# Kernel optimization log

Hardware: AMD Instinct MI355X
Metric: run time of the kernel (lower is better)

The kernel has to match this reference:

```python
import jax, jax.numpy as jnp
import numpy as np

NODE_NUM = 6
C_IN = 1024
B = 16384
N_OPS = 9
TAU = 10.0
EPS = 1e-5
ACTS = (jax.nn.relu, jax.nn.sigmoid, jnp.tanh)


def setup_inputs() -> dict:
    key = jax.random.key(0)
    k = jax.random.split(key, 12)
    n_edges = NODE_NUM * (NODE_NUM + 1) // 2  # 21
    nB = n_edges - NODE_NUM  # 15 edges with cin=cout=C_IN//2

    def w(kk, shape, fan_in):
        return jax.random.normal(kk, shape, jnp.float32) / np.float32(np.sqrt(fan_in))

    return {
        "x": jax.random.normal(k[0], (B, C_IN), jnp.float32),
        "arch_params": 0.001 * jax.random.normal(k[1], (n_edges, N_OPS), jnp.float32),
        "gumbel": jax.random.gumbel(k[2], (n_edges, N_OPS), jnp.float32),
        "dense_w_A": w(k[3], (NODE_NUM, 3, C_IN // 2, C_IN), C_IN),
        "dense_b_A": 0.01 * jax.random.normal(k[4], (NODE_NUM, 3, C_IN // 2), jnp.float32),
        "group_w_A": w(k[5], (NODE_NUM, 3, 4, C_IN // 8, C_IN // 4), C_IN // 4),
        "group_b_A": 0.01 * jax.random.normal(k[6], (NODE_NUM, 3, C_IN // 2), jnp.float32),
        "pool_w_A": w(k[7], (NODE_NUM, 2, C_IN // 2, C_IN), C_IN),
        "dense_w_B": w(k[8], (nB, 3, C_IN // 2, C_IN // 2), C_IN // 2),
        "dense_b_B": 0.01 * jax.random.normal(k[9], (nB, 3, C_IN // 2), jnp.float32),
        "group_w_B": w(k[10], (nB, 3, 4, C_IN // 8, C_IN // 8), C_IN // 8),
        "group_b_B": 0.01 * jax.random.normal(k[11], (nB, 3, C_IN // 2), jnp.float32),
    }


def _batchnorm(h):
    # training-mode BatchNorm2d on [B, C, 1, 1] == normalize over batch, affine-free
    m = jnp.mean(h, axis=0, keepdims=True)
    v = jnp.var(h, axis=0, keepdims=True)
    return (h - m) * jax.lax.rsqrt(v + EPS)


def _apply_edge(h, op_idx, wscale, dw, db, gw, gb, pw):
    # h: [B, cin]; dw: [3, cout, cin]; gw: [3, 4, cout//4, cin//4]; pw: [2, cout, cin] or None
    cout = dw.shape[1]

    def pool(p):
        def f(hh):
            # ReLU-Conv1x1-BN preprocess when cin != cout, else identity
            y = _batchnorm(jax.nn.relu(hh) @ pw[p].T) if pw is not None else hh
            if p == 0:  # avg_pool_3x3 on 1x1 spatial, pad=1, count_include_pad
                y = y / 9.0
            # p == 1: max_pool_3x3 on 1x1 spatial is identity
            return _batchnorm(y)  # MixedOp-appended BatchNorm2d(affine=False)
        return f

    def dense(a):
        return lambda hh: ACTS[a](hh @ dw[a].T + db[a])

    def gdense(a):
        def f(hh):
            hg = hh.reshape(hh.shape[0], 4, -1)  # [B, 4, cin//4]
            y = jnp.einsum('bgi,goi->bgo', hg, gw[a]).reshape(hh.shape[0], -1) + gb[a]
            return ACTS[a](y)
        return f

    zero = lambda hh: jnp.zeros((hh.shape[0], cout), hh.dtype)
    branches = [pool(0), pool(1), dense(0), dense(1), dense(2),
                gdense(0), gdense(1), gdense(2), zero]
    return jax.lax.switch(op_idx, branches, h) * wscale


def reference(x, arch_params, gumbel, dense_w_A, dense_b_A, group_w_A, group_b_A,
              pool_w_A, dense_w_B, dense_b_B, group_w_B, group_b_B):
    # GDAS gumbel-softmax hard routing (straight-through)
    logits = (jax.nn.log_softmax(arch_params, axis=1) + gumbel) / TAU
    prob = jax.nn.softmax(logits, axis=1)
    index = jnp.argmax(prob, axis=1)                      # [n_edges]
    one_h = jax.nn.one_hot(index, N_OPS, dtype=prob.dtype)
    hardwts = one_h - jax.lax.stop_gradient(prob) + prob  # [n_edges, N_OPS]

    # arch rows are indexed by sorted edge-key order, matching torch edge2index
    keys = sorted('{}->{}'.format(j, i + 1) for i in range(NODE_NUM) for j in range(i + 1))
    e2i = {kk: n for n, kk in enumerate(keys)}

    states = [x]
    a_ct = 0
    b_ct = 0
    for i in range(1, NODE_NUM + 1):
        acc = None
        for j in range(i):
            e = e2i['{}->{}'.format(j, i)]
            w_e = hardwts[e, index[e]]
            if j == 0:
                out = _apply_edge(states[0], index[e], w_e, dense_w_A[a_ct], dense_b_A[a_ct],
                                  group_w_A[a_ct], group_b_A[a_ct], pool_w_A[a_ct])
                a_ct += 1
            else:
                out = _apply_edge(states[j], index[e], w_e, dense_w_B[b_ct], dense_b_B[b_ct],
                                  group_w_B[b_ct], group_b_B[b_ct], None)
                b_ct += 1
            acc = out if acc is None else acc + out
        states.append(acc)
    return states[-1]  # [B, C_IN//2]; final_linear is never applied in forward()
```

## Files before the change

kernel.cpp:

```cpp
#include <hip/hip_runtime.h>

#define BATCH 16384
#define CH 512
#define EPSBN 1e-5f

typedef __attribute__((ext_vector_type(8))) short short8;
typedef __attribute__((ext_vector_type(4))) float f32x4;
typedef __attribute__((ext_vector_type(4))) unsigned short ushort4v;

#define GLOAD16(gp, lp) __builtin_amdgcn_global_load_lds( \
    (const __attribute__((address_space(1))) void*)(gp),  \
    (__attribute__((address_space(3))) void*)(lp), 16, 0, 0)

__constant__ int d_etab[6][6] = {
  {0,0,0,0,0,0},
  {1,6,0,0,0,0},
  {2,7,11,0,0,0},
  {3,8,12,15,0,0},
  {4,9,13,16,18,0},
  {5,10,14,17,19,20}};
__constant__ int d_bct[21] = {0,0,0,0,0,0, 0,1,3,6,10, 2,4,7,11, 5,8,12, 9,13, 14};

static __device__ __forceinline__ long woff(int e){
  return (e < 6) ? (long)e*524288 : 3145728L + (long)d_bct[e]*262144;
}

static __device__ __forceinline__ unsigned short f2b(float f){
  union { float f; unsigned u; } v; v.f = f;
  unsigned r = v.u + 0x7fffu + ((v.u >> 16) & 1u);
  return (unsigned short)(r >> 16);
}
static __device__ __forceinline__ float b2f(unsigned short u){
  union { unsigned u; float f; } v; v.u = ((unsigned)u) << 16; return v.f;
}
static __device__ __forceinline__ float actf(int act, float v){
  if (act == 0) return fmaxf(v, 0.f);
  if (act == 1) return 1.f/(1.f + __expf(-v));
  float e = __expf(2.f*v);
  return 1.f - 2.f/(e + 1.f);
}

static __device__ __forceinline__ void col_stats_atomic(
    float vs, float vq, int cn, int slot, float* partw){
  vs += __shfl_xor(vs, 16); vs += __shfl_xor(vs, 32);
  vq += __shfl_xor(vq, 16); vq += __shfl_xor(vq, 32);
  if (((threadIdx.x) & 63) < 16){
    atomicAdd(&partw[((long)slot*CH + cn)*2    ], vs);
    atomicAdd(&partw[((long)slot*CH + cn)*2 + 1], vq);
  }
}

static __device__ __forceinline__ void ms_from(const float* part, int slot, int cn,
                                               float& mu, float& var){
  long sl = ((long)slot*CH + cn)*2;
  float s = part[sl], q = part[sl+1];
  mu = s * (1.f/16384.f);
  var = fmaxf(q * (1.f/16384.f) - mu*mu, 0.f);
}
static __device__ __forceinline__ float alphaA(int id, float v){
  float s1r = rsqrtf(v + EPSBN);
  float vz = v / (v + EPSBN);
  return (id==0) ? (s1r * (1.f/9.f) * rsqrtf(vz*(1.f/81.f) + EPSBN))
                 : (s1r * rsqrtf(vz + EPSBN));
}
static __device__ __forceinline__ float alphaB(int id, float v){
  return (id==0) ? ((1.f/9.f) * rsqrtf(v*(1.f/81.f) + EPSBN))
                 : rsqrtf(v + EPSBN);
}

__global__ void k_sentinel(float* out){ out[0] = 1.0e6f; }

__global__ void k_index(const float* __restrict__ ap, const float* __restrict__ gum,
                        int* __restrict__ idx, float* __restrict__ wsc,
                        int* __restrict__ statNeed){
  __shared__ int sid[21];
  int e = threadIdx.x;
  if (e < 21){
    const float* a = ap + e*9;
    const float* g = gum + e*9;
    float m = a[0];
    for (int o=1;o<9;o++) m = fmaxf(m, a[o]);
    float s = 0.f;
    for (int o=0;o<9;o++) s += expf(a[o]-m);
    float lse = m + logf(s);
    float lg[9]; float lm = -1e30f;
    for (int o=0;o<9;o++){ lg[o] = (a[o]-lse+g[o]) / 10.0f; lm = fmaxf(lm, lg[o]); }
    float ss = 0.f;
    for (int o=0;o<9;o++) ss += expf(lg[o]-lm);
    int bi = 0; float bp = -1.f;
    for (int o=0;o<9;o++){
      float p = expf(lg[o]-lm)/ss;
      if (p > bp){ bp = p; bi = o; }
    }
    idx[e] = bi;
    wsc[e] = (1.0f - bp) + bp;
    sid[e] = bi;
  }
  __syncthreads();
  if (e < 12){
    int need = 0;
    if (e < 6){
      need = (sid[e] < 2) ? 1 : 0;
    } else {
      int j = e - 6;
      if (j >= 1){
        for (int n = j+1; n <= 6; ++n)
          if (sid[d_etab[n-1][j]] < 2) need = 1;
      }
    }
    statNeed[e] = need;
  }
}

__global__ void k_f2b4(const float* __restrict__ in, unsigned short* __restrict__ outp, long n4){
  long stride = (long)gridDim.x*blockDim.x;
  for (long i = (long)blockIdx.x*blockDim.x + threadIdx.x; i < n4; i += stride){
    const float4 v = ((const float4*)in)[i];
    ushort4v o;
    o[0] = f2b(v.x); o[1] = f2b(v.y); o[2] = f2b(v.z); o[3] = f2b(v.w);
    ((ushort4v*)outp)[i] = o;
  }
}

__global__ void k_wconv_all(const int* __restrict__ idxp,
                            const float* __restrict__ dwA, const float* __restrict__ pwA,
                            const float* __restrict__ gwA, const float* __restrict__ dwB,
                            const float* __restrict__ gwB,
                            unsigned short* __restrict__ Wball){
  int e = blockIdx.x >> 7;
  int blk = blockIdx.x & 127;
  int id = idxp[e];
  const float* src; long n;
  if (e < 6){
    int a = e;
    if (id >= 2 && id <= 4){ n = 524288; src = dwA + ((long)a*3 + (id-2))*n; }
    else if (id < 2)       { n = 524288; src = pwA + ((long)a*2 + id)*n; }
    else if (id <= 7)      { n = 131072; src = gwA + ((long)a*3 + (id-5))*131072; }
    else return;
  } else {
    int b = d_bct[e];
    if (id >= 2 && id <= 4)     { n = 262144; src = dwB + ((long)b*3 + (id-2))*n; }
    else if (id >= 5 && id <= 7){ n = 65536;  src = gwB + ((long)b*3 + (id-5))*65536; }
    else return;
  }
  unsigned short* dst = Wball + woff(e);
  long n4 = n >> 2;
  long stride = 128*256;
  for (long i = (long)blk*256 + threadIdx.x; i < n4; i += stride){
    const float4 v = ((const float4*)src)[i];
    ushort4v o;
    o[0] = f2b(v.x); o[1] = f2b(v.y); o[2] = f2b(v.z); o[3] = f2b(v.w);
    ((ushort4v*)dst)[i] = o;
  }
}

__global__ __launch_bounds__(512, 4) void k_gemmA_all(
    const unsigned short* __restrict__ xb, const unsigned short* __restrict__ Wball,
    unsigned short* __restrict__ s0, unsigned short* __restrict__ s1,
    unsigned short* __restrict__ s2, unsigned short* __restrict__ s3,
    unsigned short* __restrict__ s4, unsigned short* __restrict__ pre6,
    const float* __restrict__ dbA, const float* __restrict__ gbA,
    const int* __restrict__ idxp, const float* __restrict__ wscp,
    float* __restrict__ partw)
{
  int e = blockIdx.x >> 9;
  int id = idxp[e];
  if (id == 8) return;
  unsigned short* target;
  switch(e){ case 0: target=s0; break; case 1: target=s1; break; case 2: target=s2; break;
             case 3: target=s3; break; case 4: target=s4; break; default: target=pre6; }
  bool pool = (id < 2);
  bool grp = (id >= 5);
  int K = grp ? 256 : 1024;
  int act = pool ? 0 : (grp ? id-5 : id-2);
  float we = wscp[e];

  int inner = blockIdx.x & 511;
  int lg = (inner & 7) * 64 + (inner >> 3);
  int rowTile = lg >> 2, colTile = lg & 3;
  int row0 = rowTile * 128, col0 = colTile * 128;

  int t = threadIdx.x;
  int lane = t & 63, wave = t >> 6;
  int wm = wave >> 2, wn = wave & 3;
  int l16 = lane & 15, lq = lane >> 4;

  __shared__ unsigned short LDS[24576];

  int ra = t >> 2;
  int ca = (((t & 3) ^ ((ra >> 1) & 3)) << 3);
  int aoff[4], boff[2];
  #pragma unroll
  for (int m=0;m<4;m++){ int R = wm*64 + m*16 + l16; aoff[m] = R*32 + ((lq ^ ((R>>1)&3))<<3); }
  #pragma unroll
  for (int n=0;n<2;n++){ int C = wn*32 + n*16 + l16; boff[n] = C*32 + ((lq ^ ((C>>1)&3))<<3); }

  const unsigned short* Abase = xb + (grp ? (long)colTile*K : 0);
  const unsigned short* Wbase = Wball + (long)e*524288 + (long)col0*K;
  const unsigned short* gA = Abase + (long)(row0 + ra)*1024 + ca;
  const unsigned short* gB = Wbase + (long)ra*K + ca;
  const float* bias = (grp ? gbA : dbA) + ((long)e*3 + act)*CH;

  f32x4 acc[4][2];
  #pragma unroll
  for (int m=0;m<4;m++){ acc[m][0]=(f32x4){0,0,0,0}; acc[m][1]=(f32x4){0,0,0,0}; }

  auto STAGE = [&](int tile, int bsel){
    long kk = (long)tile*32;
    GLOAD16(gA + kk, &LDS[bsel*4096 + t*8]);
    GLOAD16(gB + kk, &LDS[12288 + bsel*4096 + t*8]);
  };

  int nk = K >> 5;
  STAGE(0, 0);
  STAGE(1, 1);
  int cb = 0;
  for (int kt = 0; kt < nk; ++kt){
    if (kt+1 < nk) { asm volatile("s_waitcnt vmcnt(2)" ::: "memory"); }
    else           { asm volatile("s_waitcnt vmcnt(0)" ::: "memory"); }
    __builtin_amdgcn_s_barrier();
    if (kt+2 < nk) STAGE(kt+2, (cb >= 1) ? cb-1 : cb+2);
    const unsigned short* pA = &LDS[cb*4096];
    const unsigned short* pB = &LDS[12288 + cb*4096];
    short8 a[4], b[2];
    #pragma unroll
    for (int m=0;m<4;m++){
      a[m] = *(const short8*)(pA + aoff[m]);
      if (pool){
        #pragma unroll
        for (int q=0;q<8;q++) a[m][q] = (a[m][q] < (short)0) ? (short)0 : a[m][q];
      }
    }
    #pragma unroll
    for (int n=0;n<2;n++) b[n] = *(const short8*)(pB + boff[n]);
    #pragma unroll
    for (int m=0;m<4;m++)
      #pragma unroll
      for (int n=0;n<2;n++)
        acc[m][n] = __builtin_amdgcn_mfma_f32_16x16x32_bf16(a[m], b[n], acc[m][n], 0,0,0);
    cb = (cb+1 == 3) ? 0 : cb+1;
  }

  #pragma unroll
  for (int n=0;n<2;n++){
    int cn = col0 + wn*32 + n*16 + l16;
    float bv = pool ? 0.f : bias[cn];
    float cs = 0.f, cq = 0.f;
    #pragma unroll
    for (int m=0;m<4;m++)
      #pragma unroll
      for (int r=0;r<4;r++){
        int row = row0 + wm*64 + m*16 + lq*4 + r;
        long off = (long)row*CH + cn;
        float v = pool ? acc[m][n][r] : (we * actf(act, acc[m][n][r] + bv));
        target[off] = f2b(v);
        cs += v; cq += v*v;
      }
    if (pool) col_stats_atomic(cs, cq, cn, e, partw);
  }
}

__global__ __launch_bounds__(512, 4) void k_fix1(
    unsigned short* __restrict__ s1, const float* __restrict__ part,
    float* __restrict__ partw, const int* __restrict__ idxp,
    const float* __restrict__ wscp, const int* __restrict__ statNeed)
{
  int id = idxp[0];
  int needS = statNeed[7];
  if (id >= 2 && id != 8 && !needS) return;
  float we = wscp[0];

  int bid = blockIdx.x;
  int lg = (bid & 7) * 64 + (bid >> 3);
  int rowTile = lg >> 2, colTile = lg & 3;
  int row0 = rowTile * 128, col0 = colTile * 128;

  int t = threadIdx.x;
  int lane = t & 63, wave = t >> 6;
  int wm = wave >> 2, wn = wave & 3;
  int l16 = lane & 15, lq = lane >> 4;

  #pragma unroll
  for (int n=0;n<2;n++){
    int cn = col0 + wn*32 + n*16 + l16;
    float cs = 0.f, cq = 0.f;
    float mu = 0.f, al = 0.f;
    if (id < 2){
      float var; ms_from(part, 0, cn, mu, var);
      al = alphaA(id, var);
    }
    #pragma unroll
    for (int m=0;m<4;m++)
      #pragma unroll
      for (int r=0;r<4;r++){
        int row = row0 + wm*64 + m*16 + lq*4 + r;
        long off = (long)row*CH + cn;
        float v;
        if (id == 8){ v = 0.f; s1[off] = 0; }
        else if (id < 2){ v = we * (b2f(s1[off]) - mu) * al; s1[off] = f2b(v); }
        else { v = b2f(s1[off]); }
        cs += v; cq += v*v;
      }
    if (needS) col_stats_atomic(cs, cq, cn, 6+1, partw);
  }
}

__global__ __launch_bounds__(512, 4) void k_fused(
    int node,
    const unsigned short* __restrict__ pre,
    const unsigned short* __restrict__ sb0, const unsigned short* __restrict__ sb1,
    const unsigned short* __restrict__ sb2, const unsigned short* __restrict__ sb3,
    const unsigned short* __restrict__ sb4,
    unsigned short* __restrict__ sbout, float* __restrict__ outf,
    const unsigned short* __restrict__ Wball,
    const float* __restrict__ dbB, const float* __restrict__ gbB,
    const float* __restrict__ part, float* __restrict__ partw,
    const int* __restrict__ idxp, const float* __restrict__ wscp,
    const int* __restrict__ statNeed)
{
  int bid = blockIdx.x;
  int lg = (bid & 7) * 64 + (bid >> 3);
  int rowTile = lg >> 2, colTile = lg & 3;
  int row0 = rowTile * 128, col0 = colTile * 128;

  int t = threadIdx.x;
  int lane = t & 63, wave = t >> 6;
  int wm = wave >> 2, wn = wave & 3;
  int l16 = lane & 15, lq = lane >> 4;

  __shared__ unsigned short LDS[24576];

  int ra = t >> 2;
  int ca = (((t & 3) ^ ((ra >> 1) & 3)) << 3);
  int aoff[4], boff[2];
  #pragma unroll
  for (int m=0;m<4;m++){ int R = wm*64 + m*16 + l16; aoff[m] = R*32 + ((lq ^ ((R>>1)&3))<<3); }
  #pragma unroll
  for (int n=0;n<2;n++){ int C = wn*32 + n*16 + l16; boff[n] = C*32 + ((lq ^ ((C>>1)&3))<<3); }

  f32x4 facc[4][2];
  #pragma unroll
  for (int m=0;m<4;m++){ facc[m][0]=(f32x4){0,0,0,0}; facc[m][1]=(f32x4){0,0,0,0}; }

  for (int jj = 0; jj < node; ++jj){
    int e = d_etab[node-1][jj];
    int id = idxp[e];
    if (id == 8) continue;
    float we = wscp[e];

    if (jj == 0){
      if (id < 2){
        #pragma unroll
        for (int n=0;n<2;n++){
          int cn = col0 + wn*32 + n*16 + l16;
          float mu, var; ms_from(part, e, cn, mu, var);
          float al = alphaA(id, var);
          #pragma unroll
          for (int m=0;m<4;m++){
            int rowb = row0 + wm*64 + m*16 + lq*4;
            #pragma unroll
            for (int r=0;r<4;r++)
              facc[m][n][r] += we * (b2f(pre[(long)(rowb+r)*CH + cn]) - mu) * al;
          }
        }
      } else {
        #pragma unroll
        for (int n=0;n<2;n++){
          int cn = col0 + wn*32 + n*16 + l16;
          #pragma unroll
          for (int m=0;m<4;m++){
            int rowb = row0 + wm*64 + m*16 + lq*4;
            #pragma unroll
            for (int r=0;r<4;r++)
              facc[m][n][r] += b2f(pre[(long)(rowb+r)*CH + cn]);
          }
        }
      }
      continue;
    }

    const unsigned short* st;
    switch(jj){ case 1: st=sb0; break; case 2: st=sb1; break;
                case 3: st=sb2; break; case 4: st=sb3; break; default: st=sb4; }

    if (id < 2){
      #pragma unroll
      for (int n=0;n<2;n++){
        int cn = col0 + wn*32 + n*16 + l16;
        float mu, var; ms_from(part, 6+jj, cn, mu, var);
        float al = alphaB(id, var);
        #pragma unroll
        for (int m=0;m<4;m++){
          int rowb = row0 + wm*64 + m*16 + lq*4;
          #pragma unroll
          for (int r=0;r<4;r++)
            facc[m][n][r] += we * (b2f(st[(long)(rowb+r)*CH + cn]) - mu) * al;
        }
      }
      continue;
    }

    bool grp = (id >= 5);
    int K = grp ? 128 : 512;
    int act = grp ? id - 5 : id - 2;
    const unsigned short* Abase = st + (grp ? (long)colTile*K : 0);
    const unsigned short* Wbase = Wball + woff(e) + (long)col0*K;
    const float* bias = (grp ? gbB : dbB) + ((long)d_bct[e]*3 + act)*CH;

    const unsigned short* gA = Abase + (long)(row0 + ra)*512 + ca;
    const unsigned short* gB = Wbase + (long)ra*K + ca;

    f32x4 acc[4][2];
    #pragma unroll
    for (int m=0;m<4;m++){ acc[m][0]=(f32x4){0,0,0,0}; acc[m][1]=(f32x4){0,0,0,0}; }

    auto STAGE = [&](int tile, int bsel){
      long kk = (long)tile*32;
      GLOAD16(gA + kk, &LDS[bsel*4096 + t*8]);
      GLOAD16(gB + kk, &LDS[12288 + bsel*4096 + t*8]);
    };

    int nk = K >> 5;
    __builtin_amdgcn_s_barrier();
    STAGE(0, 0);
    STAGE(1, 1);
    int cb = 0;
    for (int kt = 0; kt < nk; ++kt){
      if (kt+1 < nk) { asm volatile("s_waitcnt vmcnt(2)" ::: "memory"); }
      else           { asm volatile("s_waitcnt vmcnt(0)" ::: "memory"); }
      __builtin_amdgcn_s_barrier();
      if (kt+2 < nk) STAGE(kt+2, (cb >= 1) ? cb-1 : cb+2);
      const unsigned short* pA = &LDS[cb*4096];
      const unsigned short* pB = &LDS[12288 + cb*4096];
      short8 a[4], b[2];
      #pragma unroll
      for (int m=0;m<4;m++) a[m] = *(const short8*)(pA + aoff[m]);
      #pragma unroll
      for (int n=0;n<2;n++) b[n] = *(const short8*)(pB + boff[n]);
      #pragma unroll
      for (int m=0;m<4;m++)
        #pragma unroll
        for (int n=0;n<2;n++)
          acc[m][n] = __builtin_amdgcn_mfma_f32_16x16x32_bf16(a[m], b[n], acc[m][n], 0,0,0);
      cb = (cb+1 == 3) ? 0 : cb+1;
    }

    #pragma unroll
    for (int n=0;n<2;n++){
      int cn = col0 + wn*32 + n*16 + l16;
      float bv = bias[cn];
      #pragma unroll
      for (int m=0;m<4;m++)
        #pragma unroll
        for (int r=0;r<4;r++)
          facc[m][n][r] += we * actf(act, acc[m][n][r] + bv);
    }
  }

  int needS = (node < 6) ? statNeed[6+node] : 0;
  #pragma unroll
  for (int n=0;n<2;n++){
    int cn = col0 + wn*32 + n*16 + l16;
    float cs = 0.f, cq = 0.f;
    #pragma unroll
    for (int m=0;m<4;m++){
      int rowb = row0 + wm*64 + m*16 + lq*4;
      #pragma unroll
      for (int r=0;r<4;r++){
        long off = (long)(rowb+r)*CH + cn;
        float v = facc[m][n][r];
        if (node == 6) outf[off] = v;
        else { sbout[off] = f2b(v); cs += v; cq += v*v; }
      }
    }
    if (needS) col_stats_atomic(cs, cq, cn, 6+node, partw);
  }
}

extern "C" void kernel_launch(void* const* d_in, const int* in_sizes, int n_in,
                              void* d_out, int out_size, void* d_ws, size_t ws_size,
                              hipStream_t stream)
{
  const float* x   = (const float*)d_in[0];
  const float* ap  = (const float*)d_in[1];
  const float* gum = (const float*)d_in[2];
  const float* dwA = (const float*)d_in[3];
  const float* dbA = (const float*)d_in[4];
  const float* gwA = (const float*)d_in[5];
  const float* gbA = (const float*)d_in[6];
  const float* pwA = (const float*)d_in[7];
  const float* dwB = (const float*)d_in[8];
  const float* dbB = (const float*)d_in[9];
  const float* gwB = (const float*)d_in[10];
  const float* gbB = (const float*)d_in[11];
  float* out = (float*)d_out;

  char* ws = (char*)d_ws;
  size_t cur = 0;
  auto alloc = [&](size_t bytes)->void*{
    size_t o = cur; cur += (bytes + 255) & ~(size_t)255; return (void*)(ws + o);
  };
  int*   idx  = (int*)  alloc(21*sizeof(int));
  float* wsc  = (float*)alloc(21*sizeof(float));
  int*   stn  = (int*)  alloc(12*sizeof(int));
  float* part = (float*)alloc((size_t)12*CH*2*sizeof(float));
  unsigned short* Wball = (unsigned short*)alloc((size_t)7077888*sizeof(unsigned short));
  unsigned short* pre6  = (unsigned short*)alloc((size_t)BATCH*CH*sizeof(unsigned short));
  unsigned short* xb    = (unsigned short*)alloc((size_t)BATCH*1024*sizeof(unsigned short));
  unsigned short* sb[5];
  for (int i=0;i<5;i++)
    sb[i] = (unsigned short*)alloc((size_t)BATCH*CH*sizeof(unsigned short));

  if (cur > ws_size){
    hipLaunchKernelGGL(k_sentinel, dim3(1), dim3(1), 0, stream, out);
    return;
  }

  hipMemsetAsync(part, 0, (size_t)12*CH*2*sizeof(float), stream);
  hipLaunchKernelGGL(k_f2b4, dim3(2048), dim3(256), 0, stream, x, xb, (long)BATCH*1024/4);
  hipLaunchKernelGGL(k_index, dim3(1), dim3(32), 0, stream, ap, gum, idx, wsc, stn);
  hipLaunchKernelGGL(k_wconv_all, dim3(21*128), dim3(256), 0, stream,
                     idx, dwA, pwA, gwA, dwB, gwB, Wball);

  hipLaunchKernelGGL(k_gemmA_all, dim3(6*512), dim3(512), 0, stream,
                     xb, Wball, sb[0], sb[1], sb[2], sb[3], sb[4], pre6,
                     dbA, gbA, idx, wsc, part);
  hipLaunchKernelGGL(k_fix1, dim3(512), dim3(512), 0, stream,
                     sb[0], part, part, idx, wsc, stn);

  for (int node = 2; node <= 6; node++){
    const unsigned short* pre = (node < 6) ? sb[node-1] : pre6;
    unsigned short* sbout = (node < 6) ? sb[node-1] : sb[0] ;
    hipLaunchKernelGGL(k_fused, dim3(512), dim3(512), 0, stream,
                       node, pre, sb[0], sb[1], sb[2], sb[3], sb[4],
                       sbout, out, Wball, dbB, gbB, part, part, idx, wsc, stn);
  }
}
```

Baseline: 406.2 us.

## Use 256x256 tiles with 64-wide K and interleaved staging for dense GEMM A

The dense and pool edges of the A-stage GEMM (K=1024) now use 256x256 output tiles computed by 8 waves with 128x64 sub-tiles. Each K step covers 64 and is double-buffered in a 128KB LDS allocation. Global-to-LDS loads are split into chunks that are interleaved between MFMA phases, and s_setprio raises priority during MFMA. The grouped path keeps the old 128x128 kernel. The goal is more data reuse and higher MFMA density per loaded byte, at the cost of lower occupancy (launch bounds drop to 2), higher register pressure, and idle blocks in the oversized grid.

```diff
diff --git a/kernel.cpp b/kernel.cpp
--- a/kernel.cpp
+++ b/kernel.cpp
@@ -154,7 +154,7 @@
   }
 }
 
-__global__ __launch_bounds__(512, 4) void k_gemmA_all(
+__global__ __launch_bounds__(512, 2) void k_gemmA_all(
     const unsigned short* __restrict__ xb, const unsigned short* __restrict__ Wball,
     unsigned short* __restrict__ s0, unsigned short* __restrict__ s1,
     unsigned short* __restrict__ s2, unsigned short* __restrict__ s3,
@@ -163,6 +163,8 @@
     const int* __restrict__ idxp, const float* __restrict__ wscp,
     float* __restrict__ partw)
 {
+  __shared__ unsigned short LDS[65536];
+
   int e = blockIdx.x >> 9;
   int id = idxp[e];
   if (id == 8) return;
@@ -171,92 +173,243 @@
              case 3: target=s3; break; case 4: target=s4; break; default: target=pre6; }
   bool pool = (id < 2);
   bool grp = (id >= 5);
-  int K = grp ? 256 : 1024;
-  int act = pool ? 0 : (grp ? id-5 : id-2);
   float we = wscp[e];
-
   int inner = blockIdx.x & 511;
-  int lg = (inner & 7) * 64 + (inner >> 3);
-  int rowTile = lg >> 2, colTile = lg & 3;
-  int row0 = rowTile * 128, col0 = colTile * 128;
 
   int t = threadIdx.x;
   int lane = t & 63, wave = t >> 6;
-  int wm = wave >> 2, wn = wave & 3;
   int l16 = lane & 15, lq = lane >> 4;
 
-  __shared__ unsigned short LDS[24576];
-
-  int ra = t >> 2;
-  int ca = (((t & 3) ^ ((ra >> 1) & 3)) << 3);
-  int aoff[4], boff[2];
-  #pragma unroll
-  for (int m=0;m<4;m++){ int R = wm*64 + m*16 + l16; aoff[m] = R*32 + ((lq ^ ((R>>1)&3))<<3); }
-  #pragma unroll
-  for (int n=0;n<2;n++){ int C = wn*32 + n*16 + l16; boff[n] = C*32 + ((lq ^ ((C>>1)&3))<<3); }
-
-  const unsigned short* Abase = xb + (grp ? (long)colTile*K : 0);
-  const unsigned short* Wbase = Wball + (long)e*524288 + (long)col0*K;
-  const unsigned short* gA = Abase + (long)(row0 + ra)*1024 + ca;
-  const unsigned short* gB = Wbase + (long)ra*K + ca;
-  const float* bias = (grp ? gbA : dbA) + ((long)e*3 + act)*CH;
-
-  f32x4 acc[4][2];
-  #pragma unroll
-  for (int m=0;m<4;m++){ acc[m][0]=(f32x4){0,0,0,0}; acc[m][1]=(f32x4){0,0,0,0}; }
-
-  auto STAGE = [&](int tile, int bsel){
-    long kk = (long)tile*32;
-    GLOAD16(gA + kk, &LDS[bsel*4096 + t*8]);
-    GLOAD16(gB + kk, &LDS[12288 + bsel*4096 + t*8]);
-  };
-
-  int nk = K >> 5;
-  STAGE(0, 0);
-  STAGE(1, 1);
-  int cb = 0;
-  for (int kt = 0; kt < nk; ++kt){
-    if (kt+1 < nk) { asm volatile("s_waitcnt vmcnt(2)" ::: "memory"); }
-    else           { asm volatile("s_waitcnt vmcnt(0)" ::: "memory"); }
-    __builtin_amdgcn_s_barrier();
-    if (kt+2 < nk) STAGE(kt+2, (cb >= 1) ? cb-1 : cb+2);
-    const unsigned short* pA = &LDS[cb*4096];
-    const unsigned short* pB = &LDS[12288 + cb*4096];
-    short8 a[4], b[2];
-    #pragma unroll
-    for (int m=0;m<4;m++){
-      a[m] = *(const short8*)(pA + aoff[m]);
-      if (pool){
-        #pragma unroll
-        for (int q=0;q<8;q++) a[m][q] = (a[m][q] < (short)0) ? (short)0 : a[m][q];
-      }
-    }
-    #pragma unroll
-    for (int n=0;n<2;n++) b[n] = *(const short8*)(pB + boff[n]);
-    #pragma unroll
-    for (int m=0;m<4;m++)
-      #pragma unroll
-      for (int n=0;n<2;n++)
-        acc[m][n] = __builtin_amdgcn_mfma_f32_16x16x32_bf16(a[m], b[n], acc[m][n], 0,0,0);
-    cb = (cb+1 == 3) ? 0 : cb+1;
-  }
-
-  #pragma unroll
-  for (int n=0;n<2;n++){
-    int cn = col0 + wn*32 + n*16 + l16;
-    float bv = pool ? 0.f : bias[cn];
-    float cs = 0.f, cq = 0.f;
-    #pragma unroll
-    for (int m=0;m<4;m++)
-      #pragma unroll
-      for (int r=0;r<4;r++){
-        int row = row0 + wm*64 + m*16 + lq*4 + r;
-        long off = (long)row*CH + cn;
-        float v = pool ? acc[m][n][r] : (we * actf(act, acc[m][n][r] + bv));
-        target[off] = f2b(v);
-        cs += v; cq += v*v;
-      }
-    if (pool) col_stats_atomic(cs, cq, cn, e, partw);
+  if (!grp){
+    if (inner >= 128) return;
+    int act = pool ? 0 : id - 2;
+    int lg = (inner & 7) * 16 + (inner >> 3);
+    int rowTile = lg >> 1, colTile = lg & 1;
+    int row0 = rowTile * 256, col0 = colTile * 256;
+    int wm = wave >> 2, wn = wave & 3;
+
+    int srow = t >> 3;
+    int sch  = (t & 7) ^ (srow & 7);
+    const unsigned short* gA0 = xb + (long)(row0 + srow)*1024 + sch*8;
+    const unsigned short* gB0 = Wball + (long)e*524288 + (long)(col0 + srow)*1024 + sch*8;
+
+    int aoff[8][2], boff[4][2];
+    #pragma unroll
+    for (int mf=0; mf<8; mf++){
+      int R = wm*128 + mf*16 + l16;
+      #pragma unroll
+      for (int ks=0; ks<2; ks++)
+        aoff[mf][ks] = R*64 + ((((ks<<2)|lq)) ^ (R&7))*8;
+    }
+    #pragma unroll
+    for (int nf=0; nf<4; nf++){
+      int C = wn*64 + nf*16 + l16;
+      #pragma unroll
+      for (int ks=0; ks<2; ks++)
+        boff[nf][ks] = 16384 + C*64 + ((((ks<<2)|lq)) ^ (C&7))*8;
+    }
+
+    f32x4 acc[8][4];
+    #pragma unroll
+    for (int mf=0; mf<8; mf++)
+      #pragma unroll
+      for (int nf=0; nf<4; nf++) acc[mf][nf] = (f32x4){0,0,0,0};
+
+    auto STG = [&](int ld, int tile, int bb){
+      if (ld < 4)
+        GLOAD16(gA0 + (long)ld*65536 + tile*64, &LDS[bb + ld*4096 + t*8]);
+      else
+        GLOAD16(gB0 + (long)(ld-4)*65536 + tile*64, &LDS[bb + 16384 + (ld-4)*4096 + t*8]);
+    };
+
+    short8 a[4][2], bl[2][2], br[2][2];
+    auto KTILE = [&](int rdB, int stTile, int stB, bool doStage, bool drain){
+      if (doStage){ STG(0, stTile, stB); STG(1, stTile, stB); }
+      if (drain) { asm volatile("s_waitcnt vmcnt(0)" ::: "memory"); }
+      else       { asm volatile("s_waitcnt vmcnt(2)" ::: "memory"); }
+      __builtin_amdgcn_s_barrier();
+      #pragma unroll
+      for (int i=0;i<4;i++)
+        #pragma unroll
+        for (int ks=0;ks<2;ks++){
+          a[i][ks] = *(const short8*)(&LDS[rdB + aoff[i][ks]]);
+          if (pool){
+            #pragma unroll
+            for (int q=0;q<8;q++) a[i][ks][q] = (a[i][ks][q] < (short)0) ? (short)0 : a[i][ks][q];
+          }
+        }
+      #pragma unroll
+      for (int nf=0;nf<2;nf++)
+        #pragma unroll
+        for (int ks=0;ks<2;ks++)
+          bl[nf][ks] = *(const short8*)(&LDS[rdB + boff[nf][ks]]);
+      __builtin_amdgcn_s_setprio(1);
+      #pragma unroll
+      for (int i=0;i<4;i++)
+        #pragma unroll
+        for (int nf=0;nf<2;nf++){
+          acc[i][nf] = __builtin_amdgcn_mfma_f32_16x16x32_bf16(a[i][0], bl[nf][0], acc[i][nf], 0,0,0);
+          acc[i][nf] = __builtin_amdgcn_mfma_f32_16x16x32_bf16(a[i][1], bl[nf][1], acc[i][nf], 0,0,0);
+        }
+      __builtin_amdgcn_s_setprio(0);
+      __builtin_amdgcn_s_barrier();
+      if (doStage){ STG(2, stTile, stB); STG(3, stTile, stB); }
+      __builtin_amdgcn_s_barrier();
+      #pragma unroll
+      for (int nf=0;nf<2;nf++)
+        #pragma unroll
+        for (int ks=0;ks<2;ks++)
+          br[nf][ks] = *(const short8*)(&LDS[rdB + boff[2+nf][ks]]);
+      __builtin_amdgcn_s_setprio(1);
+      #pragma unroll
+      for (int i=0;i<4;i++)
+        #pragma unroll
+        for (int nf=0;nf<2;nf++){
+          acc[i][2+nf] = __builtin_amdgcn_mfma_f32_16x16x32_bf16(a[i][0], br[nf][0], acc[i][2+nf], 0,0,0);
+          acc[i][2+nf] = __builtin_amdgcn_mfma_f32_16x16x32_bf16(a[i][1], br[nf][1], acc[i][2+nf], 0,0,0);
+        }
+      __builtin_amdgcn_s_setprio(0);
+      __builtin_amdgcn_s_barrier();
+      if (doStage){ STG(4, stTile, stB); STG(5, stTile, stB); }
+      __builtin_amdgcn_s_barrier();
+      #pragma unroll
+      for (int i=0;i<4;i++)
+        #pragma unroll
+        for (int ks=0;ks<2;ks++){
+          a[i][ks] = *(const short8*)(&LDS[rdB + aoff[4+i][ks]]);
+          if (pool){
+            #pragma unroll
+            for (int q=0;q<8;q++) a[i][ks][q] = (a[i][ks][q] < (short)0) ? (short)0 : a[i][ks][q];
+          }
+        }
+      __builtin_amdgcn_s_setprio(1);
+      #pragma unroll
+      for (int i=0;i<4;i++)
+        #pragma unroll
+        for (int nf=0;nf<2;nf++){
+          acc[4+i][2+nf] = __builtin_amdgcn_mfma_f32_16x16x32_bf16(a[i][0], br[nf][0], acc[4+i][2+nf], 0,0,0);
+          acc[4+i][2+nf] = __builtin_amdgcn_mfma_f32_16x16x32_bf16(a[i][1], br[nf][1], acc[4+i][2+nf], 0,0,0);
+        }
+      __builtin_amdgcn_s_setprio(0);
+      __builtin_amdgcn_s_barrier();
+      if (doStage){ STG(6, stTile, stB); STG(7, stTile, stB); }
+      __builtin_amdgcn_s_barrier();
+      __builtin_amdgcn_s_setprio(1);
+      #pragma unroll
+      for (int i=0;i<4;i++)
+        #pragma unroll
+        for (int nf=0;nf<2;nf++){
+          acc[4+i][nf] = __builtin_amdgcn_mfma_f32_16x16x32_bf16(a[i][0], bl[nf][0], acc[4+i][nf], 0,0,0);
+          acc[4+i][nf] = __builtin_amdgcn_mfma_f32_16x16x32_bf16(a[i][1], bl[nf][1], acc[4+i][nf], 0,0,0);
+        }
+      __builtin_amdgcn_s_setprio(0);
+      __builtin_amdgcn_s_barrier();
+    };
+
+    #pragma unroll
+    for (int ld=0; ld<8; ld++) STG(ld, 0, 0);
+
+    const int niter = 8;
+    for (int tt = 0; tt < niter; ++tt){
+      KTILE(0, 2*tt+1, 32768, true, false);
+      bool more = (tt+1 < niter);
+      KTILE(32768, 2*tt+2, 0, more, !more);
+    }
+
+    const float* bias = dbA + ((long)e*3 + act)*CH;
+    #pragma unroll
+    for (int nf=0; nf<4; nf++){
+      int cn = col0 + wn*64 + nf*16 + l16;
+      float bv = pool ? 0.f : bias[cn];
+      float cs = 0.f, cq = 0.f;
+      #pragma unroll
+      for (int mf=0; mf<8; mf++)
+        #pragma unroll
+        for (int r=0;r<4;r++){
+          int row = row0 + wm*128 + mf*16 + lq*4 + r;
+          long off = (long)row*CH + cn;
+          float v = pool ? acc[mf][nf][r] : (we * actf(act, acc[mf][nf][r] + bv));
+          target[off] = f2b(v);
+          cs += v; cq += v*v;
+        }
+      if (pool) col_stats_atomic(cs, cq, cn, e, partw);
+    }
+    return;
+  }
+
+  {
+    int K = 256;
+    int act = id - 5;
+    int lg = (inner & 7) * 64 + (inner >> 3);
+    int rowTile = lg >> 2, colTile = lg & 3;
+    int row0 = rowTile * 128, col0 = colTile * 128;
+    int wm = wave >> 2, wn = wave & 3;
+
+    int ra = t >> 2;
+    int ca = (((t & 3) ^ ((ra >> 1) & 3)) << 3);
+    int aoff[4], boff[2];
+    #pragma unroll
+    for (int m=0;m<4;m++){ int R = wm*64 + m*16 + l16; aoff[m] = R*32 + ((lq ^ ((R>>1)&3))<<3); }
+    #pragma unroll
+    for (int n=0;n<2;n++){ int C = wn*32 + n*16 + l16; boff[n] = C*32 + ((lq ^ ((C>>1)&3))<<3); }
+
+    const unsigned short* Abase = xb + (long)colTile*K;
+    const unsigned short* Wbase = Wball + (long)e*524288 + (long)col0*K;
+    const unsigned short* gA = Abase + (long)(row0 + ra)*1024 + ca;
+    const unsigned short* gB = Wbase + (long)ra*K + ca;
+    const float* bias = gbA + ((long)e*3 + act)*CH;
+
+    f32x4 acc[4][2];
+    #pragma unroll
+    for (int m=0;m<4;m++){ acc[m][0]=(f32x4){0,0,0,0}; acc[m][1]=(f32x4){0,0,0,0}; }
+
+    auto STAGE = [&](int tile, int bsel){
+      long kk = (long)tile*32;
+      GLOAD16(gA + kk, &LDS[bsel*4096 + t*8]);
+      GLOAD16(gB + kk, &LDS[12288 + bsel*4096 + t*8]);
+    };
+
+    int nk = K >> 5;
+    STAGE(0, 0);
+    STAGE(1, 1);
+    int cb = 0;
+    for (int kt = 0; kt < nk; ++kt){
+      if (kt+1 < nk) { asm volatile("s_waitcnt vmcnt(2)" ::: "memory"); }
+      else           { asm volatile("s_waitcnt vmcnt(0)" ::: "memory"); }
+      __builtin_amdgcn_s_barrier();
+      if (kt+2 < nk) STAGE(kt+2, (cb >= 1) ? cb-1 : cb+2);
+      const unsigned short* pA = &LDS[cb*4096];
+      const unsigned short* pB = &LDS[12288 + cb*4096];
+      short8 a[4], b[2];
+      #pragma unroll
+      for (int m=0;m<4;m++) a[m] = *(const short8*)(pA + aoff[m]);
+      #pragma unroll
+      for (int n=0;n<2;n++) b[n] = *(const short8*)(pB + boff[n]);
+      #pragma unroll
+      for (int m=0;m<4;m++)
+        #pragma unroll
+        for (int n=0;n<2;n++)
+          acc[m][n] = __builtin_amdgcn_mfma_f32_16x16x32_bf16(a[m], b[n], acc[m][n], 0,0,0);
+      cb = (cb+1 == 3) ? 0 : cb+1;
+    }
+
+    #pragma unroll
+    for (int n=0;n<2;n++){
+      int cn = col0 + wn*32 + n*16 + l16;
+      float bv = bias[cn];
+      float cs = 0.f, cq = 0.f;
+      #pragma unroll
+      for (int m=0;m<4;m++)
+        #pragma unroll
+        for (int r=0;r<4;r++){
+          int row = row0 + wm*64 + m*16 + lq*4 + r;
+          long off = (long)row*CH + cn;
+          float v = we * actf(act, acc[m][n][r] + bv);
+          target[off] = f2b(v);
+          cs += v; cq += v*v;
+        }
+      (void)cs; (void)cq;
+    }
   }
 }
 
```

New measurement: 436.9 us. 1.08x slower.
